# Kernel tuning notes

Hardware: AMD Instinct MI355X
Metric: run time of the kernel (lower is better)

The kernel has to match this reference:

```python
import jax, jax.numpy as jnp
import numpy as np

B, S, D = 2, 2048, 2048
H, KVH, HD = 16, 4, 128
N_REP = H // KVH
SCALING = HD ** -0.5
ROPE_THETA = 10000.0


def _rope_tables(batch, seq, head_dim, dtype=jnp.float32):
    inv_freq = 1.0 / (ROPE_THETA ** (jnp.arange(0, head_dim, 2, dtype=jnp.float32) / head_dim))
    t = jnp.arange(seq, dtype=jnp.float32)
    freqs = jnp.outer(t, inv_freq)                      # [S, HD/2]
    emb = jnp.concatenate([freqs, freqs], axis=-1)      # [S, HD]
    cos = jnp.broadcast_to(jnp.cos(emb), (batch, seq, head_dim)).astype(dtype)
    sin = jnp.broadcast_to(jnp.sin(emb), (batch, seq, head_dim)).astype(dtype)
    return cos, sin


def _causal_mask(batch, seq, dtype=jnp.float32):
    # HF-style additive causal mask: 0 where allowed, large negative where masked
    neg = jnp.finfo(dtype).min
    m = jnp.triu(jnp.full((seq, seq), neg, dtype=dtype), k=1)
    return jnp.broadcast_to(m[None, None], (batch, 1, seq, seq))


def setup_inputs() -> dict:
    key = jax.random.key(0)
    ks = jax.random.split(key, 8)
    w_scale = 0.02
    hidden_states = jax.random.normal(ks[0], (B, S, D), dtype=jnp.float32)
    cos, sin = _rope_tables(B, S, HD)
    attention_mask = _causal_mask(B, S)
    # Linear weights stored as [in, out] (transposed vs torch nn.Linear.weight)
    Wq = jax.random.normal(ks[1], (D, H * HD), dtype=jnp.float32) * w_scale
    bq = jax.random.normal(ks[2], (H * HD,), dtype=jnp.float32) * w_scale
    Wk = jax.random.normal(ks[3], (D, KVH * HD), dtype=jnp.float32) * w_scale
    bk = jax.random.normal(ks[4], (KVH * HD,), dtype=jnp.float32) * w_scale
    Wv = jax.random.normal(ks[5], (D, KVH * HD), dtype=jnp.float32) * w_scale
    bv = jax.random.normal(ks[6], (KVH * HD,), dtype=jnp.float32) * w_scale
    Wo = jax.random.normal(ks[7], (H * HD, D), dtype=jnp.float32) * w_scale
    return {"hidden_states": hidden_states, "cos": cos, "sin": sin,
            "attention_mask": attention_mask, "Wq": Wq, "bq": bq,
            "Wk": Wk, "bk": bk, "Wv": Wv, "bv": bv, "Wo": Wo}


def _rotate_half(x):
    x1, x2 = jnp.split(x, 2, axis=-1)
    return jnp.concatenate([-x2, x1], axis=-1)


def reference(hidden_states, cos, sin, attention_mask, Wq, bq, Wk, bk, Wv, bv, Wo):
    b, s, _ = hidden_states.shape
    # QKV projections -> [B, heads, S, HD]
    q = (hidden_states @ Wq + bq).reshape(b, s, H, HD).transpose(0, 2, 1, 3)
    k = (hidden_states @ Wk + bk).reshape(b, s, KVH, HD).transpose(0, 2, 1, 3)
    v = (hidden_states @ Wv + bv).reshape(b, s, KVH, HD).transpose(0, 2, 1, 3)
    # RoPE (cos/sin broadcast over heads via unsqueeze_dim=1)
    c = cos[:, None]  # [B,1,S,HD]
    sn = sin[:, None]
    q = q * c + _rotate_half(q) * sn
    k = k * c + _rotate_half(k) * sn
    # GQA: repeat_interleave KV heads to match query heads
    k_rep = jnp.repeat(k, N_REP, axis=1)  # [B,H,S,HD]
    v_rep = jnp.repeat(v, N_REP, axis=1)
    # Eager attention: full score matrix, fp32 softmax
    scores = jnp.einsum('bhqd,bhkd->bhqk', q, k_rep) * SCALING + attention_mask
    attn_weights = jax.nn.softmax(scores.astype(jnp.float32), axis=-1).astype(q.dtype)
    attn_out = jnp.einsum('bhqk,bhkd->bhqd', attn_weights, v_rep)
    attn_out = attn_out.transpose(0, 2, 1, 3).reshape(b, s, H * HD)
    attn_out = attn_out @ Wo
    return attn_out, attn_weights
```

## Files before the change

kernel.cpp:

```cpp
#include <hip/hip_runtime.h>

typedef unsigned short ushort_t;
typedef __attribute__((ext_vector_type(8))) short short8;
typedef __attribute__((ext_vector_type(4))) float f32x4;

#define S_  2048
#define Dm  2048
#define NH  16
#define NKV 4
#define HD_ 128
#define C2_ 0.12751879524465536f

__device__ __forceinline__ ushort_t f2bf(float f) {
  union { float f; unsigned u; } v; v.f = f;
  unsigned u = v.u;
  return (ushort_t)((u + 0x7FFFu + ((u >> 16) & 1u)) >> 16);
}
__device__ __forceinline__ float bf2f(ushort_t h) {
  union { unsigned u; float f; } v; v.u = ((unsigned)h) << 16;
  return v.f;
}
__device__ __forceinline__ void gl_lds16(const void* g, void* l) {
  __builtin_amdgcn_global_load_lds((const __attribute__((address_space(1))) void*)g,
                                   (__attribute__((address_space(3))) void*)l, 16, 0, 0);
}

__global__ void conv_f32_bf16(const float* __restrict__ src, ushort_t* __restrict__ dst) {
  int i = blockIdx.x * 256 + threadIdx.x;
  float4 v = ((const float4*)src)[i];
  union { ushort_t u[4]; uint2 v2; } o;
  o.u[0] = f2bf(v.x); o.u[1] = f2bf(v.y); o.u[2] = f2bf(v.z); o.u[3] = f2bf(v.w);
  *(uint2*)&dst[(size_t)i * 4] = o.v2;
}

__global__ void transpose_all(const float* __restrict__ Wq, const float* __restrict__ Wk,
                              const float* __restrict__ Wv, const float* __restrict__ Wo,
                              ushort_t* __restrict__ wtqkv, ushort_t* __restrict__ wto) {
  __shared__ float tile[32][33];
  const float* src;
  ushort_t* dst;
  int N;
  switch (blockIdx.z) {
    case 0: src = Wq; dst = wtqkv; N = 2048; break;
    case 1: src = Wk; dst = wtqkv + (size_t)2048 * 2048; N = 512; break;
    case 2: src = Wv; dst = wtqkv + (size_t)2560 * 2048; N = 512; break;
    default: src = Wo; dst = wto; N = 2048; break;
  }
  int n0 = blockIdx.x * 32, k0 = blockIdx.y * 32;
  if (n0 >= N) return;
  int c = threadIdx.x & 31, r = threadIdx.x >> 5;
#pragma unroll
  for (int i = 0; i < 32; i += 8)
    tile[r + i][c] = src[(size_t)(k0 + r + i) * N + n0 + c];
  __syncthreads();
#pragma unroll
  for (int i = 0; i < 32; i += 8)
    dst[(size_t)(n0 + r + i) * 2048 + k0 + c] = f2bf(tile[c][r + i]);
}

__global__ void transpose_v(const ushort_t* __restrict__ qkv, ushort_t* __restrict__ vt) {
  __shared__ ushort_t tile[32][33];
  int b = blockIdx.z >> 2, kvh = blockIdx.z & 3;
  int s0 = blockIdx.x * 32, d0 = blockIdx.y * 32;
  int c = threadIdx.x & 31, r = threadIdx.x >> 5;
#pragma unroll
  for (int i = 0; i < 32; i += 8)
    tile[r + i][c] = qkv[(size_t)(b * S_ + s0 + r + i) * 3072 + 2560 + kvh * HD_ + d0 + c];
  __syncthreads();
#pragma unroll
  for (int i = 0; i < 32; i += 8)
    vt[(size_t)(blockIdx.z * 128 + d0 + r + i) * S_ + s0 + c] = tile[c][r + i];
}

__global__ void rope_k(ushort_t* __restrict__ qkv, const float* __restrict__ cosT,
                       const float* __restrict__ sinT) {
  int idx = blockIdx.x * 256 + threadIdx.x;
  int d = idx & 63;
  int rest = idx >> 6;
  int hh = rest % 20;
  int row = rest / 20;
  int b = row >> 11, s = row & 2047;
  int col0 = (hh < 16) ? hh * 128 : 2048 + (hh - 16) * 128;
  float c  = cosT[(size_t)(b * S_ + s) * HD_ + d];
  float sn = sinT[(size_t)(b * S_ + s) * HD_ + d];
  ushort_t* p = qkv + (size_t)row * 3072 + col0 + d;
  float v0 = bf2f(p[0]), v1 = bf2f(p[64]);
  p[0]  = f2bf(v0 * c - v1 * sn);
  p[64] = f2bf(v1 * c + v0 * sn);
}

__global__ __launch_bounds__(256, 2) void gemm_qkv_k(
    const ushort_t* __restrict__ A, const ushort_t* __restrict__ Bt, ushort_t* __restrict__ C,
    const float* __restrict__ bq, const float* __restrict__ bk2, const float* __restrict__ bv) {
  const int N = 3072, K = 2048;
  __shared__ ushort_t lA[128 * 32];
  __shared__ ushort_t lB[128 * 32];
  const int n0 = blockIdx.x * 128, m0 = blockIdx.y * 128;
  const int t = threadIdx.x;
  const int w = t >> 6, l = t & 63, lr = l & 15, lg = l >> 4;
  const int wr = w >> 1, wc = w & 1;
  const int srow = t >> 2, ssl = t & 3;

  f32x4 acc[4][4];
#pragma unroll
  for (int i = 0; i < 4; i++)
#pragma unroll
    for (int j = 0; j < 4; j++) acc[i][j] = (f32x4){0.f, 0.f, 0.f, 0.f};

  for (int kt = 0; kt < K; kt += 32) {
    {
      int r0 = srow, r1 = srow + 64;
      gl_lds16(A + (size_t)(m0 + r0) * K + kt + ((ssl ^ ((r0 >> 1) & 3)) << 3), &lA[w * 512]);
      gl_lds16(A + (size_t)(m0 + r1) * K + kt + ((ssl ^ ((r1 >> 1) & 3)) << 3), &lA[2048 + w * 512]);
      gl_lds16(Bt + (size_t)(n0 + r0) * K + kt + ((ssl ^ ((r0 >> 1) & 3)) << 3), &lB[w * 512]);
      gl_lds16(Bt + (size_t)(n0 + r1) * K + kt + ((ssl ^ ((r1 >> 1) & 3)) << 3), &lB[2048 + w * 512]);
    }
    __syncthreads();
    short8 af[4], bfr[4];
#pragma unroll
    for (int mi = 0; mi < 4; mi++) {
      int row = wr * 64 + mi * 16 + lr;
      af[mi] = *(const short8*)((const char*)lA + row * 64 + ((lg ^ ((row >> 1) & 3)) << 4));
    }
#pragma unroll
    for (int ni = 0; ni < 4; ni++) {
      int row = wc * 64 + ni * 16 + lr;
      bfr[ni] = *(const short8*)((const char*)lB + row * 64 + ((lg ^ ((row >> 1) & 3)) << 4));
    }
#pragma unroll
    for (int mi = 0; mi < 4; mi++)
#pragma unroll
      for (int ni = 0; ni < 4; ni++)
        acc[mi][ni] = __builtin_amdgcn_mfma_f32_16x16x32_bf16(af[mi], bfr[ni], acc[mi][ni], 0, 0, 0);
    __syncthreads();
  }
#pragma unroll
  for (int mi = 0; mi < 4; mi++)
#pragma unroll
    for (int ni = 0; ni < 4; ni++)
#pragma unroll
      for (int r = 0; r < 4; r++) {
        int row = m0 + wr * 64 + mi * 16 + lg * 4 + r;
        int col = n0 + wc * 64 + ni * 16 + lr;
        float bias = (col < 2048) ? bq[col] : (col < 2560) ? bk2[col - 2048] : bv[col - 2560];
        C[(size_t)row * N + col] = f2bf(acc[mi][ni][r] + bias);
      }
}

__global__ __launch_bounds__(256, 2) void attn_k(
    const ushort_t* __restrict__ qkv, const ushort_t* __restrict__ vt,
    float* __restrict__ linv_g, ushort_t* __restrict__ attnO) {
  __shared__ ushort_t lK[2][64 * 128];
  __shared__ ushort_t lV[2][128 * 64];
  __shared__ ushort_t lP[4][16 * 64];
  const int pairI = blockIdx.x, h = blockIdx.y, b = blockIdx.z;
  const int kvh = h >> 2;
  const int t = threadIdx.x, w = t >> 6, l = t & 63, lr = l & 15, lg = l >> 4;
  ushort_t* lPw = lP[w];

  auto stage = [&](int kt, int bufi) {
#pragma unroll
    for (int c = 0; c < 4; c++) {
      int row = c * 16 + (t >> 4), sl = t & 15;
      gl_lds16(qkv + (size_t)(b * S_ + kt * 64 + row) * 3072 + 2048 + kvh * HD_ +
                   ((sl ^ (row & 15)) << 3),
               &lK[bufi][c * 2048 + w * 512]);
    }
#pragma unroll
    for (int c = 0; c < 4; c++) {
      int row = c * 32 + (t >> 3), sl = t & 7;
      gl_lds16(vt + (size_t)((b * 4 + kvh) * 128 + row) * S_ + kt * 64 +
                   ((sl ^ (row & 7)) << 3),
               &lV[bufi][c * 2048 + w * 512]);
    }
  };

  for (int sel = 0; sel < 2; sel++) {
    const int qt = sel ? (31 - pairI) : pairI;
    const int qw = qt * 64 + w * 16;
    const int nkt = qt + 1;

    short8 qf[4];
#pragma unroll
    for (int kc = 0; kc < 4; kc++)
      qf[kc] = *(const short8*)&qkv[(size_t)(b * S_ + qw + lr) * 3072 + h * HD_ + kc * 32 + lg * 8];

    float lsum[4];
    f32x4 o[8];
#pragma unroll
    for (int r = 0; r < 4; r++) lsum[r] = 0.f;
#pragma unroll
    for (int dj = 0; dj < 8; dj++) o[dj] = (f32x4){0.f, 0.f, 0.f, 0.f};

    stage(0, 0);
    for (int kt = 0; kt < nkt; kt++) {
      const int cur = kt & 1;
      if (kt + 1 < nkt) {
        stage(kt + 1, cur ^ 1);
        asm volatile("s_waitcnt vmcnt(8)" ::: "memory");
      } else {
        asm volatile("s_waitcnt vmcnt(0)" ::: "memory");
      }
      __builtin_amdgcn_s_barrier();

      f32x4 s[4];
#pragma unroll
      for (int ni = 0; ni < 4; ni++) s[ni] = (f32x4){0.f, 0.f, 0.f, 0.f};
#pragma unroll
      for (int kc = 0; kc < 4; kc++) {
        short8 kf[4];
#pragma unroll
        for (int ni = 0; ni < 4; ni++) {
          int row = ni * 16 + lr;
          kf[ni] = *(const short8*)((const char*)lK[cur] + row * 256 +
                                    (((kc * 4 + lg) ^ (row & 15)) << 4));
        }
#pragma unroll
        for (int ni = 0; ni < 4; ni++)
          s[ni] = __builtin_amdgcn_mfma_f32_16x16x32_bf16(qf[kc], kf[ni], s[ni], 0, 0, 0);
      }

      const bool diag = (kt == nkt - 1);
#pragma unroll
      for (int ni = 0; ni < 4; ni++)
#pragma unroll
        for (int r = 0; r < 4; r++) {
          float p = exp2f(s[ni][r] * C2_);
          if (diag) {
            int colg = kt * 64 + ni * 16 + lr;
            int rowg = qw + lg * 4 + r;
            if (colg > rowg) p = 0.f;
          }
          lsum[r] += p;
          int rowl = lg * 4 + r;
          int col = ni * 16 + lr;
          lPw[rowl * 64 + (((col >> 3) ^ (rowl & 7)) << 3) + (col & 7)] = f2bf(p);
        }

#pragma unroll
      for (int kc = 0; kc < 2; kc++) {
        short8 pa;
        {
          int row = lr;
          pa = *(const short8*)((const char*)lPw + row * 128 + (((kc * 4 + lg) ^ (row & 7)) << 4));
        }
#pragma unroll
        for (int dj = 0; dj < 8; dj++) {
          int row = dj * 16 + lr;
          short8 vb = *(const short8*)((const char*)lV[cur] + row * 128 +
                                       (((kc * 4 + lg) ^ (row & 7)) << 4));
          o[dj] = __builtin_amdgcn_mfma_f32_16x16x32_bf16(pa, vb, o[dj], 0, 0, 0);
        }
      }
      __builtin_amdgcn_s_barrier();
    }

    float inv_l[4];
#pragma unroll
    for (int r = 0; r < 4; r++) {
      float sum = lsum[r];
#pragma unroll
      for (int off = 1; off < 16; off <<= 1) sum += __shfl_xor(sum, off);
      inv_l[r] = 1.f / sum;
      if (lr == 0) linv_g[(size_t)(b * NH + h) * S_ + qw + lg * 4 + r] = inv_l[r];
    }
#pragma unroll
    for (int dj = 0; dj < 8; dj++)
#pragma unroll
      for (int r = 0; r < 4; r++) {
        int rowg = b * S_ + qw + lg * 4 + r;
        int colg = h * HD_ + dj * 16 + lr;
        attnO[(size_t)rowg * Dm + colg] = f2bf(o[dj][r] * inv_l[r]);
      }
  }
}

__global__ __launch_bounds__(256, 2) void tail_k(
    const ushort_t* __restrict__ A, const ushort_t* __restrict__ Bt, float* __restrict__ outO,
    const ushort_t* __restrict__ qkv, const float* __restrict__ linv,
    float* __restrict__ outW) {
  __shared__ ushort_t sh[2][64 * 128];
  const int bx = blockIdx.x;
  const int t = threadIdx.x;
  const int w = t >> 6, l = t & 63, lr = l & 15, lg = l >> 4;

  if (bx < 512) {
    ushort_t* lA = sh[0];
    ushort_t* lB = sh[0] + 4096;
    const int N = 2048, K = 2048;
    const int n0 = (bx & 15) * 128, m0 = (bx >> 4) * 128;
    const int wr = w >> 1, wc = w & 1;
    const int srow = t >> 2, ssl = t & 3;

    f32x4 acc[4][4];
#pragma unroll
    for (int i = 0; i < 4; i++)
#pragma unroll
      for (int j = 0; j < 4; j++) acc[i][j] = (f32x4){0.f, 0.f, 0.f, 0.f};

    for (int kt = 0; kt < K; kt += 32) {
      {
        int r0 = srow, r1 = srow + 64;
        gl_lds16(A + (size_t)(m0 + r0) * K + kt + ((ssl ^ ((r0 >> 1) & 3)) << 3), &lA[w * 512]);
        gl_lds16(A + (size_t)(m0 + r1) * K + kt + ((ssl ^ ((r1 >> 1) & 3)) << 3),
                 &lA[2048 + w * 512]);
        gl_lds16(Bt + (size_t)(n0 + r0) * K + kt + ((ssl ^ ((r0 >> 1) & 3)) << 3), &lB[w * 512]);
        gl_lds16(Bt + (size_t)(n0 + r1) * K + kt + ((ssl ^ ((r1 >> 1) & 3)) << 3),
                 &lB[2048 + w * 512]);
      }
      __syncthreads();
      short8 af[4], bfr[4];
#pragma unroll
      for (int mi = 0; mi < 4; mi++) {
        int row = wr * 64 + mi * 16 + lr;
        af[mi] = *(const short8*)((const char*)lA + row * 64 + ((lg ^ ((row >> 1) & 3)) << 4));
      }
#pragma unroll
      for (int ni = 0; ni < 4; ni++) {
        int row = wc * 64 + ni * 16 + lr;
        bfr[ni] = *(const short8*)((const char*)lB + row * 64 + ((lg ^ ((row >> 1) & 3)) << 4));
      }
#pragma unroll
      for (int mi = 0; mi < 4; mi++)
#pragma unroll
        for (int ni = 0; ni < 4; ni++)
          acc[mi][ni] =
              __builtin_amdgcn_mfma_f32_16x16x32_bf16(af[mi], bfr[ni], acc[mi][ni], 0, 0, 0);
      __syncthreads();
    }
#pragma unroll
    for (int mi = 0; mi < 4; mi++)
#pragma unroll
      for (int ni = 0; ni < 4; ni++)
#pragma unroll
        for (int r = 0; r < 4; r++) {
          int row = m0 + wr * 64 + mi * 16 + lg * 4 + r;
          int col = n0 + wc * 64 + ni * 16 + lr;
          outO[(size_t)row * N + col] = acc[mi][ni][r];
        }
    return;
  }

  const int pid = bx - 512;
  const int bh = pid >> 4;
  const int pi = pid & 15;
  const int b = bh >> 4, h = bh & 15;
  const int kvh = h >> 2;

  auto stageK = [&](int kt, int bufi) {
#pragma unroll
    for (int c = 0; c < 4; c++) {
      int row = c * 16 + (t >> 4), sl = t & 15;
      gl_lds16(qkv + (size_t)(b * S_ + kt * 64 + row) * 3072 + 2048 + kvh * HD_ +
                   ((sl ^ (row & 15)) << 3),
               &sh[bufi][c * 2048 + w * 512]);
    }
  };

  for (int sel = 0; sel < 2; sel++) {
    const int qt = sel ? (31 - pi) : pi;
    const int qw = qt * 64 + w * 16;
    const int nkt = qt + 1;

    short8 qf[4];
#pragma unroll
    for (int kc = 0; kc < 4; kc++)
      qf[kc] = *(const short8*)&qkv[(size_t)(b * S_ + qw + lr) * 3072 + h * HD_ + kc * 32 + lg * 8];

    float invr[4];
#pragma unroll
    for (int r = 0; r < 4; r++) invr[r] = linv[(size_t)bh * S_ + qw + lg * 4 + r];

    stageK(0, 0);
    for (int kt = 0; kt < nkt; kt++) {
      const int cur = kt & 1;
      if (kt + 1 < nkt) {
        stageK(kt + 1, cur ^ 1);
        asm volatile("s_waitcnt vmcnt(4)" ::: "memory");
      } else {
        asm volatile("s_waitcnt vmcnt(0)" ::: "memory");
      }
      __builtin_amdgcn_s_barrier();

      f32x4 s[4];
#pragma unroll
      for (int ni = 0; ni < 4; ni++) s[ni] = (f32x4){0.f, 0.f, 0.f, 0.f};
#pragma unroll
      for (int kc = 0; kc < 4; kc++) {
        short8 kf[4];
#pragma unroll
        for (int ni = 0; ni < 4; ni++) {
          int row = ni * 16 + lr;
          kf[ni] = *(const short8*)((const char*)sh[cur] + row * 256 +
                                    (((kc * 4 + lg) ^ (row & 15)) << 4));
        }
#pragma unroll
        for (int ni = 0; ni < 4; ni++)
          s[ni] = __builtin_amdgcn_mfma_f32_16x16x32_bf16(qf[kc], kf[ni], s[ni], 0, 0, 0);
      }

      const bool diag = (kt == nkt - 1);
#pragma unroll
      for (int ni = 0; ni < 4; ni++)
#pragma unroll
        for (int r = 0; r < 4; r++) {
          int colg = kt * 64 + ni * 16 + lr;
          int rowg = qw + lg * 4 + r;
          float p = exp2f(s[ni][r] * C2_) * invr[r];
          if (diag && colg > rowg) p = 0.f;
          outW[((size_t)bh * S_ + rowg) * S_ + colg] = p;
        }
      __builtin_amdgcn_s_barrier();
    }

    {
      const int zc0 = nkt * 64;
      const int zn = (S_ - zc0) >> 2;
      f32x4 z = {0.f, 0.f, 0.f, 0.f};
      for (int rr = 0; rr < 16; rr++) {
        f32x4* base = (f32x4*)&outW[((size_t)bh * S_ + qt * 64 + w * 16 + rr) * S_ + zc0];
        for (int cc = l; cc < zn; cc += 64) base[cc] = z;
      }
    }
  }
}

extern "C" void kernel_launch(void* const* d_in, const int* in_sizes, int n_in,
                              void* d_out, int out_size, void* d_ws, size_t ws_size,
                              hipStream_t stream) {
  const float* hs   = (const float*)d_in[0];
  const float* cosT = (const float*)d_in[1];
  const float* sinT = (const float*)d_in[2];
  const float* Wq = (const float*)d_in[4];
  const float* bq = (const float*)d_in[5];
  const float* Wk = (const float*)d_in[6];
  const float* bk = (const float*)d_in[7];
  const float* Wv = (const float*)d_in[8];
  const float* bv = (const float*)d_in[9];
  const float* Wo = (const float*)d_in[10];

  char* ws = (char*)d_ws;
  ushort_t* hsb   = (ushort_t*)(ws);
  ushort_t* wtqkv = (ushort_t*)(ws + 16777216);
  ushort_t* wto   = (ushort_t*)(ws + 29360128);
  ushort_t* qkv   = (ushort_t*)(ws + 37748736);
  ushort_t* vt    = (ushort_t*)(ws + 62914560);
  float*    linv  = (float*)(ws + 67108864);
  ushort_t* attn  = (ushort_t*)(ws);

  float* outO = (float*)d_out;
  float* outW = outO + (size_t)8388608;

  conv_f32_bf16<<<8192, 256, 0, stream>>>(hs, hsb);
  transpose_all<<<dim3(64, 64, 4), 256, 0, stream>>>(Wq, Wk, Wv, Wo, wtqkv, wto);
  gemm_qkv_k<<<dim3(24, 32), 256, 0, stream>>>(hsb, wtqkv, qkv, bq, bk, bv);
  rope_k<<<20480, 256, 0, stream>>>(qkv, cosT, sinT);
  transpose_v<<<dim3(64, 4, 8), 256, 0, stream>>>(qkv, vt);
  attn_k<<<dim3(16, 16, 2), 256, 0, stream>>>(qkv, vt, linv, attn);
  tail_k<<<1024, 256, 0, stream>>>(attn, wto, outO, qkv, linv, outW);
}
```

Baseline: 351.8 us.

## Fuse prep and RoPE kernels, double-buffer GEMMs, XCD-aware block remapping

Merges the hidden-state conversion and weight transpose into one launch and folds RoPE into the QKV GEMM epilogue, exchanging rotate-half partners through LDS. Both GEMMs get double-buffered LDS staging with explicit vmcnt waits and raw barriers so the next tile loads while the current one computes. Block indices in the GEMMs and the attention kernel are remapped so that neighbouring work lands on the same chiplet for L2 reuse. The diagonal-mask branch in attention is hoisted out of the inner loop. This cuts launches and one full pass over QKV, at the cost of more LDS per block and extra barriers in the epilogue.

```diff
diff --git a/kernel.cpp b/kernel.cpp
--- a/kernel.cpp
+++ b/kernel.cpp
@@ -25,28 +25,32 @@
                                    (__attribute__((address_space(3))) void*)l, 16, 0, 0);
 }
 
-__global__ void conv_f32_bf16(const float* __restrict__ src, ushort_t* __restrict__ dst) {
-  int i = blockIdx.x * 256 + threadIdx.x;
-  float4 v = ((const float4*)src)[i];
-  union { ushort_t u[4]; uint2 v2; } o;
-  o.u[0] = f2bf(v.x); o.u[1] = f2bf(v.y); o.u[2] = f2bf(v.z); o.u[3] = f2bf(v.w);
-  *(uint2*)&dst[(size_t)i * 4] = o.v2;
-}
-
-__global__ void transpose_all(const float* __restrict__ Wq, const float* __restrict__ Wk,
-                              const float* __restrict__ Wv, const float* __restrict__ Wo,
-                              ushort_t* __restrict__ wtqkv, ushort_t* __restrict__ wto) {
+__global__ void prep_k(const float* __restrict__ hs, ushort_t* __restrict__ hsb,
+                       const float* __restrict__ Wq, const float* __restrict__ Wk,
+                       const float* __restrict__ Wv, const float* __restrict__ Wo,
+                       ushort_t* __restrict__ wtqkv, ushort_t* __restrict__ wto) {
   __shared__ float tile[32][33];
+  const int id = blockIdx.x;
+  if (id < 8192) {
+    int i = id * 256 + threadIdx.x;
+    float4 v = ((const float4*)hs)[i];
+    union { ushort_t u[4]; uint2 v2; } o;
+    o.u[0] = f2bf(v.x); o.u[1] = f2bf(v.y); o.u[2] = f2bf(v.z); o.u[3] = f2bf(v.w);
+    *(uint2*)&hsb[(size_t)i * 4] = o.v2;
+    return;
+  }
+  const int id2 = id - 8192;
+  const int z = id2 >> 12, ky = (id2 >> 6) & 63, nx = id2 & 63;
   const float* src;
   ushort_t* dst;
   int N;
-  switch (blockIdx.z) {
+  switch (z) {
     case 0: src = Wq; dst = wtqkv; N = 2048; break;
     case 1: src = Wk; dst = wtqkv + (size_t)2048 * 2048; N = 512; break;
     case 2: src = Wv; dst = wtqkv + (size_t)2560 * 2048; N = 512; break;
     default: src = Wo; dst = wto; N = 2048; break;
   }
-  int n0 = blockIdx.x * 32, k0 = blockIdx.y * 32;
+  int n0 = nx * 32, k0 = ky * 32;
   if (n0 >= N) return;
   int c = threadIdx.x & 31, r = threadIdx.x >> 5;
 #pragma unroll
@@ -72,79 +76,110 @@
     vt[(size_t)(blockIdx.z * 128 + d0 + r + i) * S_ + s0 + c] = tile[c][r + i];
 }
 
-__global__ void rope_k(ushort_t* __restrict__ qkv, const float* __restrict__ cosT,
-                       const float* __restrict__ sinT) {
-  int idx = blockIdx.x * 256 + threadIdx.x;
-  int d = idx & 63;
-  int rest = idx >> 6;
-  int hh = rest % 20;
-  int row = rest / 20;
-  int b = row >> 11, s = row & 2047;
-  int col0 = (hh < 16) ? hh * 128 : 2048 + (hh - 16) * 128;
-  float c  = cosT[(size_t)(b * S_ + s) * HD_ + d];
-  float sn = sinT[(size_t)(b * S_ + s) * HD_ + d];
-  ushort_t* p = qkv + (size_t)row * 3072 + col0 + d;
-  float v0 = bf2f(p[0]), v1 = bf2f(p[64]);
-  p[0]  = f2bf(v0 * c - v1 * sn);
-  p[64] = f2bf(v1 * c + v0 * sn);
-}
-
 __global__ __launch_bounds__(256, 2) void gemm_qkv_k(
     const ushort_t* __restrict__ A, const ushort_t* __restrict__ Bt, ushort_t* __restrict__ C,
-    const float* __restrict__ bq, const float* __restrict__ bk2, const float* __restrict__ bv) {
+    const float* __restrict__ bq, const float* __restrict__ bk2, const float* __restrict__ bv,
+    const float* __restrict__ cosT, const float* __restrict__ sinT) {
   const int N = 3072, K = 2048;
-  __shared__ ushort_t lA[128 * 32];
-  __shared__ ushort_t lB[128 * 32];
-  const int n0 = blockIdx.x * 128, m0 = blockIdx.y * 128;
+  __shared__ ushort_t lA[2][128 * 32];
+  __shared__ ushort_t lB[2][128 * 32];
+  const int lin = blockIdx.x;
+  const int nid = (lin & 7) * 96 + (lin >> 3);
+  const int n0 = (nid % 24) * 128, m0 = (nid / 24) * 128;
   const int t = threadIdx.x;
   const int w = t >> 6, l = t & 63, lr = l & 15, lg = l >> 4;
   const int wr = w >> 1, wc = w & 1;
   const int srow = t >> 2, ssl = t & 3;
 
+  auto stage = [&](int kt, int bufi) {
+    int r0 = srow, r1 = srow + 64;
+    gl_lds16(A + (size_t)(m0 + r0) * K + kt + ((ssl ^ ((r0 >> 1) & 3)) << 3), &lA[bufi][w * 512]);
+    gl_lds16(A + (size_t)(m0 + r1) * K + kt + ((ssl ^ ((r1 >> 1) & 3)) << 3),
+             &lA[bufi][2048 + w * 512]);
+    gl_lds16(Bt + (size_t)(n0 + r0) * K + kt + ((ssl ^ ((r0 >> 1) & 3)) << 3), &lB[bufi][w * 512]);
+    gl_lds16(Bt + (size_t)(n0 + r1) * K + kt + ((ssl ^ ((r1 >> 1) & 3)) << 3),
+             &lB[bufi][2048 + w * 512]);
+  };
+
   f32x4 acc[4][4];
 #pragma unroll
   for (int i = 0; i < 4; i++)
 #pragma unroll
     for (int j = 0; j < 4; j++) acc[i][j] = (f32x4){0.f, 0.f, 0.f, 0.f};
 
-  for (int kt = 0; kt < K; kt += 32) {
-    {
-      int r0 = srow, r1 = srow + 64;
-      gl_lds16(A + (size_t)(m0 + r0) * K + kt + ((ssl ^ ((r0 >> 1) & 3)) << 3), &lA[w * 512]);
-      gl_lds16(A + (size_t)(m0 + r1) * K + kt + ((ssl ^ ((r1 >> 1) & 3)) << 3), &lA[2048 + w * 512]);
-      gl_lds16(Bt + (size_t)(n0 + r0) * K + kt + ((ssl ^ ((r0 >> 1) & 3)) << 3), &lB[w * 512]);
-      gl_lds16(Bt + (size_t)(n0 + r1) * K + kt + ((ssl ^ ((r1 >> 1) & 3)) << 3), &lB[2048 + w * 512]);
-    }
-    __syncthreads();
+  stage(0, 0);
+  const int nit = K / 32;
+  for (int it = 0; it < nit; it++) {
+    const int cur = it & 1;
+    if (it + 1 < nit) {
+      stage((it + 1) * 32, cur ^ 1);
+      asm volatile("s_waitcnt vmcnt(4)" ::: "memory");
+    } else {
+      asm volatile("s_waitcnt vmcnt(0)" ::: "memory");
+    }
+    __builtin_amdgcn_s_barrier();
     short8 af[4], bfr[4];
 #pragma unroll
     for (int mi = 0; mi < 4; mi++) {
       int row = wr * 64 + mi * 16 + lr;
-      af[mi] = *(const short8*)((const char*)lA + row * 64 + ((lg ^ ((row >> 1) & 3)) << 4));
+      af[mi] = *(const short8*)((const char*)lA[cur] + row * 64 + ((lg ^ ((row >> 1) & 3)) << 4));
     }
 #pragma unroll
     for (int ni = 0; ni < 4; ni++) {
       int row = wc * 64 + ni * 16 + lr;
-      bfr[ni] = *(const short8*)((const char*)lB + row * 64 + ((lg ^ ((row >> 1) & 3)) << 4));
+      bfr[ni] = *(const short8*)((const char*)lB[cur] + row * 64 + ((lg ^ ((row >> 1) & 3)) << 4));
     }
 #pragma unroll
     for (int mi = 0; mi < 4; mi++)
 #pragma unroll
       for (int ni = 0; ni < 4; ni++)
         acc[mi][ni] = __builtin_amdgcn_mfma_f32_16x16x32_bf16(af[mi], bfr[ni], acc[mi][ni], 0, 0, 0);
-    __syncthreads();
-  }
-#pragma unroll
-  for (int mi = 0; mi < 4; mi++)
+    __builtin_amdgcn_s_barrier();
+  }
+
+  const bool isV = (n0 >= 2560);
+  float* fbuf = (float*)&lA[0][0];
+  const int pw_ = w ^ 1;
+#pragma unroll
+  for (int mi = 0; mi < 4; mi++) {
+    float vv[4][4];
+#pragma unroll
+    for (int ni = 0; ni < 4; ni++)
+#pragma unroll
+      for (int r = 0; r < 4; r++) {
+        int col = n0 + wc * 64 + ni * 16 + lr;
+        float bias = (col < 2048) ? bq[col] : (col < 2560) ? bk2[col - 2048] : bv[col - 2560];
+        vv[ni][r] = acc[mi][ni][r] + bias;
+      }
+    if (!isV) {
+      __syncthreads();
+#pragma unroll
+      for (int ni = 0; ni < 4; ni++)
+#pragma unroll
+        for (int r = 0; r < 4; r++)
+          fbuf[w * 1024 + (lg * 4 + r) * 64 + ni * 16 + lr] = vv[ni][r];
+      __syncthreads();
+#pragma unroll
+      for (int ni = 0; ni < 4; ni++)
+#pragma unroll
+        for (int r = 0; r < 4; r++) {
+          float pv = fbuf[pw_ * 1024 + (lg * 4 + r) * 64 + ni * 16 + lr];
+          int row = m0 + wr * 64 + mi * 16 + lg * 4 + r;
+          int d = wc * 64 + ni * 16 + lr;
+          float c = cosT[(size_t)row * HD_ + d];
+          float sn = sinT[(size_t)row * HD_ + d];
+          vv[ni][r] = (wc == 0) ? vv[ni][r] * c - pv * sn : vv[ni][r] * c + pv * sn;
+        }
+    }
 #pragma unroll
     for (int ni = 0; ni < 4; ni++)
 #pragma unroll
       for (int r = 0; r < 4; r++) {
         int row = m0 + wr * 64 + mi * 16 + lg * 4 + r;
         int col = n0 + wc * 64 + ni * 16 + lr;
-        float bias = (col < 2048) ? bq[col] : (col < 2560) ? bk2[col - 2048] : bv[col - 2560];
-        C[(size_t)row * N + col] = f2bf(acc[mi][ni][r] + bias);
-      }
+        C[(size_t)row * N + col] = f2bf(vv[ni][r]);
+      }
+  }
 }
 
 __global__ __launch_bounds__(256, 2) void attn_k(
@@ -153,7 +188,8 @@
   __shared__ ushort_t lK[2][64 * 128];
   __shared__ ushort_t lV[2][128 * 64];
   __shared__ ushort_t lP[4][16 * 64];
-  const int pairI = blockIdx.x, h = blockIdx.y, b = blockIdx.z;
+  const int nid = (blockIdx.x & 7) * 64 + (blockIdx.x >> 3);
+  const int pairI = nid & 15, h = (nid >> 4) & 15, b = nid >> 8;
   const int kvh = h >> 2;
   const int t = threadIdx.x, w = t >> 6, l = t & 63, lr = l & 15, lg = l >> 4;
   ushort_t* lPw = lP[w];
@@ -220,22 +256,30 @@
           s[ni] = __builtin_amdgcn_mfma_f32_16x16x32_bf16(qf[kc], kf[ni], s[ni], 0, 0, 0);
       }
 
-      const bool diag = (kt == nkt - 1);
-#pragma unroll
-      for (int ni = 0; ni < 4; ni++)
-#pragma unroll
-        for (int r = 0; r < 4; r++) {
-          float p = exp2f(s[ni][r] * C2_);
-          if (diag) {
+      if (kt == nkt - 1) {
+#pragma unroll
+        for (int ni = 0; ni < 4; ni++)
+#pragma unroll
+          for (int r = 0; r < 4; r++) {
+            float p = exp2f(s[ni][r] * C2_);
             int colg = kt * 64 + ni * 16 + lr;
             int rowg = qw + lg * 4 + r;
             if (colg > rowg) p = 0.f;
+            lsum[r] += p;
+            int rowl = lg * 4 + r, col = ni * 16 + lr;
+            lPw[rowl * 64 + (((col >> 3) ^ (rowl & 7)) << 3) + (col & 7)] = f2bf(p);
           }
-          lsum[r] += p;
-          int rowl = lg * 4 + r;
-          int col = ni * 16 + lr;
-          lPw[rowl * 64 + (((col >> 3) ^ (rowl & 7)) << 3) + (col & 7)] = f2bf(p);
-        }
+      } else {
+#pragma unroll
+        for (int ni = 0; ni < 4; ni++)
+#pragma unroll
+          for (int r = 0; r < 4; r++) {
+            float p = exp2f(s[ni][r] * C2_);
+            lsum[r] += p;
+            int rowl = lg * 4 + r, col = ni * 16 + lr;
+            lPw[rowl * 64 + (((col >> 3) ^ (rowl & 7)) << 3) + (col & 7)] = f2bf(p);
+          }
+      }
 
 #pragma unroll
       for (int kc = 0; kc < 2; kc++) {
@@ -285,40 +329,52 @@
   const int w = t >> 6, l = t & 63, lr = l & 15, lg = l >> 4;
 
   if (bx < 512) {
-    ushort_t* lA = sh[0];
-    ushort_t* lB = sh[0] + 4096;
     const int N = 2048, K = 2048;
-    const int n0 = (bx & 15) * 128, m0 = (bx >> 4) * 128;
+    const int nid = (bx & 7) * 64 + (bx >> 3);
+    const int n0 = (nid & 15) * 128, m0 = (nid >> 4) * 128;
     const int wr = w >> 1, wc = w & 1;
     const int srow = t >> 2, ssl = t & 3;
 
+    auto stageG = [&](int kt, int bufi) {
+      int r0 = srow, r1 = srow + 64;
+      gl_lds16(A + (size_t)(m0 + r0) * K + kt + ((ssl ^ ((r0 >> 1) & 3)) << 3), &sh[bufi][w * 512]);
+      gl_lds16(A + (size_t)(m0 + r1) * K + kt + ((ssl ^ ((r1 >> 1) & 3)) << 3),
+               &sh[bufi][2048 + w * 512]);
+      gl_lds16(Bt + (size_t)(n0 + r0) * K + kt + ((ssl ^ ((r0 >> 1) & 3)) << 3),
+               &sh[bufi][4096 + w * 512]);
+      gl_lds16(Bt + (size_t)(n0 + r1) * K + kt + ((ssl ^ ((r1 >> 1) & 3)) << 3),
+               &sh[bufi][4096 + 2048 + w * 512]);
+    };
+
     f32x4 acc[4][4];
 #pragma unroll
     for (int i = 0; i < 4; i++)
 #pragma unroll
       for (int j = 0; j < 4; j++) acc[i][j] = (f32x4){0.f, 0.f, 0.f, 0.f};
 
-    for (int kt = 0; kt < K; kt += 32) {
-      {
-        int r0 = srow, r1 = srow + 64;
-        gl_lds16(A + (size_t)(m0 + r0) * K + kt + ((ssl ^ ((r0 >> 1) & 3)) << 3), &lA[w * 512]);
-        gl_lds16(A + (size_t)(m0 + r1) * K + kt + ((ssl ^ ((r1 >> 1) & 3)) << 3),
-                 &lA[2048 + w * 512]);
-        gl_lds16(Bt + (size_t)(n0 + r0) * K + kt + ((ssl ^ ((r0 >> 1) & 3)) << 3), &lB[w * 512]);
-        gl_lds16(Bt + (size_t)(n0 + r1) * K + kt + ((ssl ^ ((r1 >> 1) & 3)) << 3),
-                 &lB[2048 + w * 512]);
-      }
-      __syncthreads();
+    stageG(0, 0);
+    const int nit = K / 32;
+    for (int it = 0; it < nit; it++) {
+      const int cur = it & 1;
+      if (it + 1 < nit) {
+        stageG((it + 1) * 32, cur ^ 1);
+        asm volatile("s_waitcnt vmcnt(4)" ::: "memory");
+      } else {
+        asm volatile("s_waitcnt vmcnt(0)" ::: "memory");
+      }
+      __builtin_amdgcn_s_barrier();
       short8 af[4], bfr[4];
 #pragma unroll
       for (int mi = 0; mi < 4; mi++) {
         int row = wr * 64 + mi * 16 + lr;
-        af[mi] = *(const short8*)((const char*)lA + row * 64 + ((lg ^ ((row >> 1) & 3)) << 4));
+        af[mi] =
+            *(const short8*)((const char*)&sh[cur][0] + row * 64 + ((lg ^ ((row >> 1) & 3)) << 4));
       }
 #pragma unroll
       for (int ni = 0; ni < 4; ni++) {
         int row = wc * 64 + ni * 16 + lr;
-        bfr[ni] = *(const short8*)((const char*)lB + row * 64 + ((lg ^ ((row >> 1) & 3)) << 4));
+        bfr[ni] = *(const short8*)((const char*)&sh[cur][4096] + row * 64 +
+                                   ((lg ^ ((row >> 1) & 3)) << 4));
       }
 #pragma unroll
       for (int mi = 0; mi < 4; mi++)
@@ -326,7 +382,7 @@
         for (int ni = 0; ni < 4; ni++)
           acc[mi][ni] =
               __builtin_amdgcn_mfma_f32_16x16x32_bf16(af[mi], bfr[ni], acc[mi][ni], 0, 0, 0);
-      __syncthreads();
+      __builtin_amdgcn_s_barrier();
     }
 #pragma unroll
     for (int mi = 0; mi < 4; mi++)
@@ -341,9 +397,10 @@
     return;
   }
 
-  const int pid = bx - 512;
-  const int bh = pid >> 4;
-  const int pi = pid & 15;
+  const int lin = bx - 512;
+  const int nid = (lin & 7) * 64 + (lin >> 3);
+  const int bh = nid >> 4;
+  const int pi = nid & 15;
   const int b = bh >> 4, h = bh & 15;
   const int kvh = h >> 2;
 
@@ -451,11 +508,9 @@
   float* outO = (float*)d_out;
   float* outW = outO + (size_t)8388608;
 
-  conv_f32_bf16<<<8192, 256, 0, stream>>>(hs, hsb);
-  transpose_all<<<dim3(64, 64, 4), 256, 0, stream>>>(Wq, Wk, Wv, Wo, wtqkv, wto);
-  gemm_qkv_k<<<dim3(24, 32), 256, 0, stream>>>(hsb, wtqkv, qkv, bq, bk, bv);
-  rope_k<<<20480, 256, 0, stream>>>(qkv, cosT, sinT);
+  prep_k<<<8192 + 16384, 256, 0, stream>>>(hs, hsb, Wq, Wk, Wv, Wo, wtqkv, wto);
+  gemm_qkv_k<<<768, 256, 0, stream>>>(hsb, wtqkv, qkv, bq, bk, bv, cosT, sinT);
   transpose_v<<<dim3(64, 4, 8), 256, 0, stream>>>(qkv, vt);
-  attn_k<<<dim3(16, 16, 2), 256, 0, stream>>>(qkv, vt, linv, attn);
+  attn_k<<<512, 256, 0, stream>>>(qkv, vt, linv, attn);
   tail_k<<<1024, 256, 0, stream>>>(attn, wto, outO, qkv, linv, outW);
 }
```

After: 341.0 us. 3.1% less time.
